# Optimization experiments

Hardware: AMD Instinct MI355X
Metric: run time of the kernel (lower is better)

## Reference

```python
import jax, jax.numpy as jnp
import numpy as np

NEG = -1e16  # matches torch masked_fill value
LN_EPS = 1e-5


def _gat_layer(h, mask, b):
    """h: [..., N, D]; mask: broadcastable bool [..., N, N]; b: broadcastable [..., D]."""
    scores = jnp.einsum('...nd,...md->...nm', h, h)
    scores = jnp.where(mask, scores, NEG)
    attn = jax.nn.softmax(scores, axis=-1)
    return jnp.einsum('...nm,...md->...nd', attn, h) + b


def setup_inputs() -> dict:
    key = jax.random.key(0)
    ks = jax.random.split(key, 6)
    B, N, C, H, D = 8, 2048, 64, 4, 64
    x = jax.random.normal(ks[0], (B, N, C), dtype=jnp.float32)
    graph = jax.random.randint(ks[1], (N, N), 0, 2, dtype=jnp.int32)
    # xavier_uniform-style scale for W: bound = sqrt(6/(fan_in+fan_out))
    bnd_h = float(np.sqrt(6.0 / (C + D)))
    Wh = jax.random.uniform(ks[2], (H, D, C), jnp.float32, -bnd_h, bnd_h)
    bh = jnp.zeros((H, D), jnp.float32)
    bnd_o = float(np.sqrt(6.0 / (H * D + D)))
    Wo = jax.random.uniform(ks[3], (D, H * D), jnp.float32, -bnd_o, bnd_o)
    bo = jnp.zeros((D,), jnp.float32)
    gamma = jnp.ones((D,), jnp.float32)
    beta = jnp.zeros((D,), jnp.float32)
    return {"x": x, "graph": graph, "Wh": Wh, "bh": bh, "Wo": Wo,
            "bo": bo, "gamma": gamma, "beta": beta}


def reference(x, graph, Wh, bh, Wo, bo, gamma, beta):
    B, N, C = x.shape
    H, D, _ = Wh.shape
    # graph = (graph + I) > 0
    mask = (graph + jnp.eye(N, dtype=graph.dtype)) > 0  # [N, N] bool
    # per-head linear projection: [B, H, N, D]
    h = jnp.einsum('bnc,hdc->bhnd', x, Wh)
    out_h = _gat_layer(h, mask[None, None], bh[None, :, None, :])  # [B,H,N,D]
    # torch.cat over heads along last dim == head-major reshape
    cat = jnp.transpose(out_h, (0, 2, 1, 3)).reshape(B, N, H * D)
    z = jax.nn.leaky_relu(cat, negative_slope=0.2)
    h2 = jnp.einsum('bnk,dk->bnd', z, Wo)  # [B, N, D]
    out2 = _gat_layer(h2, mask[None], bo)
    z2 = jax.nn.leaky_relu(out2, negative_slope=0.2)
    # LayerNorm over last dim
    mu = jnp.mean(z2, axis=-1, keepdims=True)
    var = jnp.mean(jnp.square(z2 - mu), axis=-1, keepdims=True)
    out = (z2 - mu) * jax.lax.rsqrt(var + LN_EPS) * gamma + beta
    return out  # dropout p=0.0 -> identity
```

## Files before the change

kernel.cpp:

```cpp
#include <hip/hip_runtime.h>

#define NN 2048
#define PITCH 72
#define MPITCH 264

typedef __attribute__((ext_vector_type(8))) _Float16 half8;
typedef __attribute__((ext_vector_type(4))) float floatx4;

static_assert(sizeof(half8) == 16, "");

#define MRINIT -3.0e38f

__device__ __forceinline__ unsigned short f2h(float f) {
    union { _Float16 h; unsigned short u; } v;
    v.h = (_Float16)f;
    return v.u;
}
__device__ __forceinline__ float h2f(unsigned short u) {
    union { unsigned short u; _Float16 h; } v;
    v.u = u;
    return (float)v.h;
}
__device__ __forceinline__ unsigned int pk2h(float a, float b) {
    union { __fp16 __attribute__((ext_vector_type(2))) h; unsigned int u; } v;
    v.h = __builtin_amdgcn_cvt_pkrtz(a, b);
    return v.u;
}
__device__ __forceinline__ void barrier_lds_only() {
    __asm__ __volatile__("" ::: "memory");
    __builtin_amdgcn_s_waitcnt(0xC07F);
    __builtin_amdgcn_s_barrier();
    __asm__ __volatile__("" ::: "memory");
}

__global__ __launch_bounds__(256) void mask_kernel(const int* __restrict__ graph,
                                                   unsigned int* __restrict__ mbits) {
    const int t = threadIdx.x;
    const int lane = t & 63;
    const int W = (blockIdx.x << 2) + (t >> 6);
    const int i = W >> 5;
    const int cb = W & 31;
    const int j = (cb << 6) + lane;
    const int g = graph[(size_t)i * NN + j];
    const unsigned long long bal = __ballot((g > 0) || (i == j));
    if (lane == 0)  mbits[(i << 6) + (cb << 1)]     = (unsigned int)bal;
    if (lane == 32) mbits[(i << 6) + (cb << 1) + 1] = (unsigned int)(bal >> 32);
}

__global__ __launch_bounds__(256) void proj_kernel(const float* __restrict__ x,
                                                   const float* __restrict__ Wh,
                                                   unsigned short* __restrict__ hout) {
    __shared__ float xs[16 * 64];
    __shared__ float wsh[64 * 65];
    const int t = threadIdx.x;
    const int pair = blockIdx.x >> 7;
    const int nt = blockIdx.x & 127;
    const int n0 = nt << 4;
    const int b = pair >> 2;
    const int hh = pair & 3;
    const float* xb = x + (((size_t)b * NN + n0) << 6);
    for (int i = t; i < 1024; i += 256) xs[i] = xb[i];
    const float* wb = Wh + (hh << 12);
    for (int i = t; i < 4096; i += 256) wsh[(i >> 6) * 65 + (i & 63)] = wb[i];
    __syncthreads();
    const int d = t & 63;
    const int q = t >> 6;
    float a0 = 0.f, a1 = 0.f, a2 = 0.f, a3 = 0.f;
    for (int c = 0; c < 64; ++c) {
        const float w = wsh[d * 65 + c];
        a0 += xs[(((q << 2) + 0) << 6) + c] * w;
        a1 += xs[(((q << 2) + 1) << 6) + c] * w;
        a2 += xs[(((q << 2) + 2) << 6) + c] * w;
        a3 += xs[(((q << 2) + 3) << 6) + c] * w;
    }
    unsigned short* ho = hout + (((size_t)pair * NN + n0 + (q << 2)) << 6) + d;
    ho[0]   = f2h(a0);
    ho[64]  = f2h(a1);
    ho[128] = f2h(a2);
    ho[192] = f2h(a3);
}

template <int QG, int OUTMODE>
__global__ __launch_bounds__(256) void gat_flash(const unsigned short* __restrict__ Hm,
                                                 const unsigned int* __restrict__ mbits,
                                                 const float* __restrict__ bias,
                                                 const int bias_mod,
                                                 const float* __restrict__ gamma,
                                                 const float* __restrict__ beta,
                                                 void* __restrict__ OutP,
                                                 float2* __restrict__ mlP) {
    __shared__ unsigned short Ks[2][64 * PITCH];
    __shared__ unsigned short Kts[2][64 * PITCH];
    __shared__ unsigned short Ps[4 * QG * 16 * PITCH];

    const int t = threadIdx.x;
    const int wave = t >> 6;
    const int lane = t & 63;
    const int quad = lane >> 4;
    const int m = lane & 15;

    const int qtbits = (QG == 2) ? 4 : 5;
    const int bid = blockIdx.x;
    const int qt = bid & ((1 << qtbits) - 1);
    const int split = (OUTMODE == 2) ? ((bid >> qtbits) & 1) : 0;
    const int mat = bid >> (qtbits + ((OUTMODE == 2) ? 1 : 0));
    const int q0 = qt << ((QG == 2) ? 7 : 6);
    const int nkt = (OUTMODE == 2) ? 16 : 32;
    const int kt0 = split * nkt;

    const unsigned short* Hb = Hm + ((size_t)mat << 17);
    const int wbase = q0 + wave * (16 * QG);

    const _Float16 LOG2E = (_Float16)1.44269504f;
    half8 bq0[QG], bq1[QG];
    int gq[QG];
#pragma unroll
    for (int g = 0; g < QG; ++g) {
        gq[g] = wbase + (g << 4) + m;
        bq0[g] = *(const half8*)(Hb + (gq[g] << 6) + (quad << 3)) * LOG2E;
        bq1[g] = *(const half8*)(Hb + (gq[g] << 6) + 32 + (quad << 3)) * LOG2E;
    }

    const int boff = (mat % bias_mod) << 6;
    const float bv0 = bias[boff + m];
    const float bv1 = bias[boff + 16 + m];
    const float bv2 = bias[boff + 32 + m];
    const float bv3 = bias[boff + 48 + m];

    const int p = t >> 3;
    const int cc = t & 7;
    const int jch = p >> 2;
    const int jo = (p & 3) << 1;

    float mr[QG], lr[QG];
    floatx4 O[QG][4];
#pragma unroll
    for (int g = 0; g < QG; ++g) {
        mr[g] = MRINIT;
        lr[g] = 0.f;
#pragma unroll
        for (int nt = 0; nt < 4; ++nt) O[g][nt] = floatx4{0.f, 0.f, 0.f, 0.f};
    }

    const int msw = m & 7;
    int psb[QG];
#pragma unroll
    for (int g = 0; g < QG; ++g) psb[g] = (wave * QG + g) * 1152 + m * PITCH;

    const unsigned short* kg0 = Hb + (((kt0 << 6) + (p << 1)) << 6) + (cc << 3);
    half8 ra = *(const half8*)(kg0);
    half8 rb = *(const half8*)(kg0 + 64);

    for (int it = 0; it < nkt; ++it) {
        const int kt = kt0 + it;
        unsigned short* KS = Ks[it & 1];
        unsigned short* KT = Kts[it & 1];
        *(half8*)(&KS[(p << 1) * PITCH + (cc << 3)]) = ra;
        *(half8*)(&KS[((p << 1) + 1) * PITCH + (cc << 3)]) = rb;
        union { half8 v; unsigned int u[4]; } kaU, kbU;
        kaU.v = ra;
        kbU.v = rb;
#pragma unroll
        for (int c = 0; c < 4; ++c) {
            const unsigned int ua = kaU.u[c];
            const unsigned int ub = kbU.u[c];
            const unsigned int lo = __builtin_amdgcn_perm(ub, ua, 0x05040100);
            const unsigned int hi = __builtin_amdgcn_perm(ub, ua, 0x07060302);
            const int d0 = (cc << 3) + (c << 1);
            const int pos = (((jch + cc) & 7) << 3) + jo;
            *(unsigned int*)(&KT[d0 * PITCH + pos]) = lo;
            *(unsigned int*)(&KT[(d0 + 1) * PITCH + pos]) = hi;
        }
        const int ktn = kt0 + ((it + 1) & (nkt - 1));
        const unsigned short* kgn = Hb + (((ktn << 6) + (p << 1)) << 6) + (cc << 3);
        ra = *(const half8*)(kgn);
        rb = *(const half8*)(kgn + 64);

        barrier_lds_only();

        floatx4 a[QG][4];
#pragma unroll
        for (int jt = 0; jt < 4; ++jt) {
            const half8 k0 = *(const half8*)(&KS[((jt << 4) + m) * PITCH + (quad << 3)]);
            const half8 k1 = *(const half8*)(&KS[((jt << 4) + m) * PITCH + 32 + (quad << 3)]);
#pragma unroll
            for (int g = 0; g < QG; ++g) {
                floatx4 z = {0.f, 0.f, 0.f, 0.f};
                z = __builtin_amdgcn_mfma_f32_16x16x32_f16(k0, bq0[g], z, 0, 0, 0);
                z = __builtin_amdgcn_mfma_f32_16x16x32_f16(k1, bq1[g], z, 0, 0, 0);
                a[g][jt] = z;
            }
        }

#pragma unroll
        for (int g = 0; g < QG; ++g) {
            const int mrow = gq[g] << 6;
            const unsigned int w0 = mbits[mrow + (kt << 1)];
            const unsigned int w1 = mbits[mrow + (kt << 1) + 1];

            float tmx = MRINIT;
#pragma unroll
            for (int jt = 0; jt < 4; ++jt) {
                const unsigned int wv = (jt < 2) ? w0 : w1;
                const unsigned int bits = (wv >> (((jt & 1) << 4) + (quad << 2))) & 0xFu;
#pragma unroll
                for (int reg = 0; reg < 4; ++reg) {
                    const float v = ((bits >> reg) & 1u) ? a[g][jt][reg] : MRINIT;
                    a[g][jt][reg] = v;
                    tmx = fmaxf(tmx, v);
                }
            }
            tmx = fmaxf(tmx, __shfl_xor(tmx, 16));
            tmx = fmaxf(tmx, __shfl_xor(tmx, 32));
            const float mnew = fmaxf(mr[g], tmx);
            const float alpha = __builtin_amdgcn_exp2f(mr[g] - mnew);
            const bool need = __any(mnew > mr[g]);

            float psum = 0.f;
#pragma unroll
            for (int jt = 0; jt < 4; ++jt) {
                const float p0 = __builtin_amdgcn_exp2f(a[g][jt][0] - mnew);
                const float p1 = __builtin_amdgcn_exp2f(a[g][jt][1] - mnew);
                const float p2 = __builtin_amdgcn_exp2f(a[g][jt][2] - mnew);
                const float p3 = __builtin_amdgcn_exp2f(a[g][jt][3] - mnew);
                psum += (p0 + p1) + (p2 + p3);
                const int ch = (jt << 1) + (quad >> 1);
                *(uint2*)(&Ps[psb[g] + (((ch + msw) & 7) << 3) + ((quad & 1) << 2)]) =
                    make_uint2(pk2h(p0, p1), pk2h(p2, p3));
            }
            psum += __shfl_xor(psum, 16);
            psum += __shfl_xor(psum, 32);
            lr[g] = lr[g] * alpha + psum;
            mr[g] = mnew;

            if (need) {
                const float aO0 = __shfl(alpha, (quad << 2) + 0);
                const float aO1 = __shfl(alpha, (quad << 2) + 1);
                const float aO2 = __shfl(alpha, (quad << 2) + 2);
                const float aO3 = __shfl(alpha, (quad << 2) + 3);
#pragma unroll
                for (int nt = 0; nt < 4; ++nt) {
                    O[g][nt][0] *= aO0;
                    O[g][nt][1] *= aO1;
                    O[g][nt][2] *= aO2;
                    O[g][nt][3] *= aO3;
                }
            }
        }

        __builtin_amdgcn_wave_barrier();
        __asm__ __volatile__("" ::: "memory");

        half8 pa0[QG], pa1[QG];
#pragma unroll
        for (int g = 0; g < QG; ++g) {
            pa0[g] = *(const half8*)(&Ps[psb[g] + (((quad + msw) & 7) << 3)]);
            pa1[g] = *(const half8*)(&Ps[psb[g] + (((4 + quad + msw) & 7) << 3)]);
        }
#pragma unroll
        for (int nt = 0; nt < 4; ++nt) {
            const int d = (nt << 4) + m;
            const int sw = (d >> 3) & 7;
            const half8 v0 = *(const half8*)(&KT[d * PITCH + (((quad + sw) & 7) << 3)]);
            const half8 v1 = *(const half8*)(&KT[d * PITCH + (((4 + quad + sw) & 7) << 3)]);
#pragma unroll
            for (int g = 0; g < QG; ++g) {
                O[g][nt] = __builtin_amdgcn_mfma_f32_16x16x32_f16(pa0[g], v0, O[g][nt], 0, 0, 0);
                O[g][nt] = __builtin_amdgcn_mfma_f32_16x16x32_f16(pa1[g], v1, O[g][nt], 0, 0, 0);
            }
        }
    }

    if (OUTMODE == 2) {
        float* Ob = (float*)OutP +
                    ((((size_t)(split << 3) + mat) * NN + wbase + (quad << 2)) << 6) + m;
#pragma unroll
        for (int reg = 0; reg < 4; ++reg)
#pragma unroll
            for (int nt = 0; nt < 4; ++nt)
                Ob[(reg << 6) + (nt << 4)] = O[0][nt][reg];
        if (lane < 16)
            mlP[((size_t)(split << 3) + mat) * NN + wbase + m] = make_float2(mr[0], lr[0]);
        return;
    }

    float g0, g1, g2, g3, be0, be1, be2, be3;
    if (OUTMODE == 1) {
        g0 = gamma[m]; g1 = gamma[16 + m]; g2 = gamma[32 + m]; g3 = gamma[48 + m];
        be0 = beta[m]; be1 = beta[16 + m]; be2 = beta[32 + m]; be3 = beta[48 + m];
    }
#pragma unroll
    for (int g = 0; g < QG; ++g) {
        const float l0 = 1.f / __shfl(lr[g], (quad << 2) + 0);
        const float l1 = 1.f / __shfl(lr[g], (quad << 2) + 1);
        const float l2 = 1.f / __shfl(lr[g], (quad << 2) + 2);
        const float l3 = 1.f / __shfl(lr[g], (quad << 2) + 3);
        const size_t obase = (((size_t)mat * NN + wbase + (g << 4) + (quad << 2)) << 6) + m;
#pragma unroll
        for (int reg = 0; reg < 4; ++reg) {
            const float li = (reg == 0) ? l0 : (reg == 1) ? l1 : (reg == 2) ? l2 : l3;
            float z0 = O[g][0][reg] * li + bv0;
            float z1 = O[g][1][reg] * li + bv1;
            float z2 = O[g][2][reg] * li + bv2;
            float z3 = O[g][3][reg] * li + bv3;
            z0 = (z0 > 0.f) ? z0 : 0.2f * z0;
            z1 = (z1 > 0.f) ? z1 : 0.2f * z1;
            z2 = (z2 > 0.f) ? z2 : 0.2f * z2;
            z3 = (z3 > 0.f) ? z3 : 0.2f * z3;
            if (OUTMODE == 0) {
                unsigned short* op = (unsigned short*)OutP + obase + ((size_t)reg << 6);
                op[0] = f2h(z0); op[16] = f2h(z1); op[32] = f2h(z2); op[48] = f2h(z3);
            } else {
                float s = ((z0 + z1) + (z2 + z3));
                float sq = ((z0 * z0 + z1 * z1) + (z2 * z2 + z3 * z3));
#pragma unroll
                for (int off = 1; off < 16; off <<= 1) {
                    s += __shfl_xor(s, off);
                    sq += __shfl_xor(sq, off);
                }
                const float mu = s * 0.015625f;
                float var = sq * 0.015625f - mu * mu;
                var = fmaxf(var, 0.f);
                const float rstd = rsqrtf(var + 1e-5f);
                float* op = (float*)OutP + obase + ((size_t)reg << 6);
                op[0]  = (z0 - mu) * rstd * g0 + be0;
                op[16] = (z1 - mu) * rstd * g1 + be1;
                op[32] = (z2 - mu) * rstd * g2 + be2;
                op[48] = (z3 - mu) * rstd * g3 + be3;
            }
        }
    }
}

__global__ __launch_bounds__(256) void mix_gemm(const unsigned short* __restrict__ oh,
                                                const float* __restrict__ Wo,
                                                unsigned short* __restrict__ h2) {
    __shared__ unsigned short zs[64 * MPITCH];
    __shared__ unsigned short wsm[64 * MPITCH];
    const int t = threadIdx.x;
    const int b = blockIdx.x >> 5;
    const int n0 = (blockIdx.x & 31) << 6;
    for (int i = t; i < 2048; i += 256) {
        const int hh = i >> 9;
        const int r = (i >> 3) & 63;
        const int d8 = i & 7;
        const half8 v = *(const half8*)(oh + ((((size_t)b << 2) + hh) * NN + n0 + r) * 64 + (d8 << 3));
        *(half8*)(&zs[r * MPITCH + (hh << 6) + (d8 << 3)]) = v;
    }
    for (int i = t; i < 2048; i += 256) {
        const int d = i >> 5;
        const int k0 = (i & 31) << 3;
        const float4 f0 = *(const float4*)(Wo + (d << 8) + k0);
        const float4 f1 = *(const float4*)(Wo + (d << 8) + k0 + 4);
        uint4 pk;
        pk.x = pk2h(f0.x, f0.y);
        pk.y = pk2h(f0.z, f0.w);
        pk.z = pk2h(f1.x, f1.y);
        pk.w = pk2h(f1.z, f1.w);
        *(uint4*)(&wsm[d * MPITCH + k0]) = pk;
    }
    __syncthreads();
    const int wave = t >> 6;
    const int m = t & 15;
    const int quad = (t >> 4) & 3;
    const int ar = (wave << 4) + m;
    floatx4 acc[4] = {{0.f, 0.f, 0.f, 0.f}, {0.f, 0.f, 0.f, 0.f},
                      {0.f, 0.f, 0.f, 0.f}, {0.f, 0.f, 0.f, 0.f}};
#pragma unroll
    for (int chunk = 0; chunk < 8; ++chunk) {
        const int k0 = chunk << 5;
        const half8 af = *(const half8*)(&zs[ar * MPITCH + k0 + (quad << 3)]);
#pragma unroll
        for (int nt = 0; nt < 4; ++nt) {
            const half8 bf = *(const half8*)(&wsm[((nt << 4) + m) * MPITCH + k0 + (quad << 3)]);
            acc[nt] = __builtin_amdgcn_mfma_f32_16x16x32_f16(af, bf, acc[nt], 0, 0, 0);
        }
    }
    unsigned short* hp = h2 + (((size_t)b * NN + n0 + (wave << 4) + (quad << 2)) << 6) + m;
#pragma unroll
    for (int reg = 0; reg < 4; ++reg)
#pragma unroll
        for (int nt = 0; nt < 4; ++nt)
            hp[(reg << 6) + (nt << 4)] = f2h(acc[nt][reg]);
}

__global__ __launch_bounds__(256) void combine_ln(const float* __restrict__ Opart,
                                                  const float2* __restrict__ ml,
                                                  const float* __restrict__ bo,
                                                  const float* __restrict__ gamma,
                                                  const float* __restrict__ beta,
                                                  float* __restrict__ out) {
    const int t = threadIdx.x;
    const int lane = t & 63;
    const int widx = (blockIdx.x << 2) + (t >> 6);
    const size_t r0 = (size_t)widx;
    const float2 s0 = ml[r0];
    const float2 s1 = ml[(size_t)(NN * 8) + r0];
    const float mm = fmaxf(s0.x, s1.x);
    const float c0 = __builtin_amdgcn_exp2f(s0.x - mm);
    const float c1 = __builtin_amdgcn_exp2f(s1.x - mm);
    const float l = s0.y * c0 + s1.y * c1;
    const float o0 = Opart[(r0 << 6) + lane];
    const float o1 = Opart[(((size_t)(NN * 8) + r0) << 6) + lane];
    float v = (o0 * c0 + o1 * c1) / l + bo[lane];
    v = (v > 0.f) ? v : 0.2f * v;
    float s = v;
    float sq = v * v;
#pragma unroll
    for (int off = 1; off < 64; off <<= 1) {
        s += __shfl_xor(s, off);
        sq += __shfl_xor(sq, off);
    }
    const float mu = s * 0.015625f;
    float var = sq * 0.015625f - mu * mu;
    var = fmaxf(var, 0.f);
    const float rstd = rsqrtf(var + 1e-5f);
    out[(r0 << 6) + lane] = (v - mu) * rstd * gamma[lane] + beta[lane];
}

extern "C" void kernel_launch(void* const* d_in, const int* in_sizes, int n_in,
                              void* d_out, int out_size, void* d_ws, size_t ws_size,
                              hipStream_t stream) {
    const float* x     = (const float*)d_in[0];
    const int*   graph = (const int*)d_in[1];
    const float* Wh    = (const float*)d_in[2];
    const float* bh    = (const float*)d_in[3];
    const float* Wo    = (const float*)d_in[4];
    const float* bo    = (const float*)d_in[5];
    const float* gamma = (const float*)d_in[6];
    const float* beta  = (const float*)d_in[7];
    float* out = (float*)d_out;

    char* ws = (char*)d_ws;
    unsigned int* mbits = (unsigned int*)ws;
    unsigned short* h   = (unsigned short*)(ws + 0x080000);
    unsigned short* oh  = (unsigned short*)(ws + 0x880000);
    unsigned short* h2  = (unsigned short*)(ws + 0x080000);
    float2* ml          = (float2*)(ws + 0x280000);
    float* Opart        = (float*)(ws + 0x880000);

    mask_kernel<<<16384, 256, 0, stream>>>(graph, mbits);
    proj_kernel<<<4096, 256, 0, stream>>>(x, Wh, h);
    gat_flash<2, 0><<<512, 256, 0, stream>>>(h, mbits, bh, 4, nullptr, nullptr, oh, nullptr);
    mix_gemm<<<256, 256, 0, stream>>>(oh, Wo, h2);
    gat_flash<1, 2><<<512, 256, 0, stream>>>(h2, mbits, bo, 1, nullptr, nullptr, Opart, ml);
    combine_ln<<<4096, 256, 0, stream>>>(Opart, ml, bo, gamma, beta, out);
}
```

Before: 219.8 us.

## Replace scalar projection kernel with fp16 MFMA GEMM and unpad P tile

Rewrites the per-head input projection as an MFMA-based GEMM: each block loads 64 rows of x and all four heads' weights into shared memory as fp16, and each wave computes one head with 16x16x32 MFMA instructions. The grid shrinks from 4096 to 256 blocks and x is read once per block for all heads instead of once per head. Separately, the P staging buffer in the attention kernel drops its padded pitch of 72 for a pitch of 64, which saves shared memory but may add bank conflicts unless the existing swizzle covers it. Converting x and W to fp16 before the projection changes rounding relative to the fp32 accumulation used before.

```diff
diff --git a/kernel.cpp b/kernel.cpp
--- a/kernel.cpp
+++ b/kernel.cpp
@@ -47,37 +47,68 @@
     if (lane == 32) mbits[(i << 6) + (cb << 1) + 1] = (unsigned int)(bal >> 32);
 }
 
-__global__ __launch_bounds__(256) void proj_kernel(const float* __restrict__ x,
-                                                   const float* __restrict__ Wh,
-                                                   unsigned short* __restrict__ hout) {
-    __shared__ float xs[16 * 64];
-    __shared__ float wsh[64 * 65];
+__global__ __launch_bounds__(256) void proj_gemm(const float* __restrict__ x,
+                                                 const float* __restrict__ Wh,
+                                                 unsigned short* __restrict__ hout) {
+    __shared__ unsigned short xs[64 * PITCH];
+    __shared__ unsigned short wh[4 * 64 * PITCH];
     const int t = threadIdx.x;
-    const int pair = blockIdx.x >> 7;
-    const int nt = blockIdx.x & 127;
-    const int n0 = nt << 4;
-    const int b = pair >> 2;
-    const int hh = pair & 3;
-    const float* xb = x + (((size_t)b * NN + n0) << 6);
-    for (int i = t; i < 1024; i += 256) xs[i] = xb[i];
-    const float* wb = Wh + (hh << 12);
-    for (int i = t; i < 4096; i += 256) wsh[(i >> 6) * 65 + (i & 63)] = wb[i];
+    const int b = blockIdx.x >> 5;
+    const int n0 = (blockIdx.x & 31) << 6;
+    for (int i = t; i < 512; i += 256) {
+        const int r = i >> 3, c8 = (i & 7) << 3;
+        const float* xp = x + (((size_t)b * NN + n0 + r) << 6) + c8;
+        const float4 f0 = *(const float4*)(xp);
+        const float4 f1 = *(const float4*)(xp + 4);
+        uint4 pk;
+        pk.x = pk2h(f0.x, f0.y); pk.y = pk2h(f0.z, f0.w);
+        pk.z = pk2h(f1.x, f1.y); pk.w = pk2h(f1.z, f1.w);
+        *(uint4*)(&xs[r * PITCH + c8]) = pk;
+    }
+    for (int i = t; i < 2048; i += 256) {
+        const int hd = i >> 3, c8 = (i & 7) << 3;
+        const float* wp = Wh + ((size_t)hd << 6) + c8;
+        const float4 f0 = *(const float4*)(wp);
+        const float4 f1 = *(const float4*)(wp + 4);
+        uint4 pk;
+        pk.x = pk2h(f0.x, f0.y); pk.y = pk2h(f0.z, f0.w);
+        pk.z = pk2h(f1.x, f1.y); pk.w = pk2h(f1.z, f1.w);
+        *(uint4*)(&wh[hd * PITCH + c8]) = pk;
+    }
     __syncthreads();
-    const int d = t & 63;
-    const int q = t >> 6;
-    float a0 = 0.f, a1 = 0.f, a2 = 0.f, a3 = 0.f;
-    for (int c = 0; c < 64; ++c) {
-        const float w = wsh[d * 65 + c];
-        a0 += xs[(((q << 2) + 0) << 6) + c] * w;
-        a1 += xs[(((q << 2) + 1) << 6) + c] * w;
-        a2 += xs[(((q << 2) + 2) << 6) + c] * w;
-        a3 += xs[(((q << 2) + 3) << 6) + c] * w;
-    }
-    unsigned short* ho = hout + (((size_t)pair * NN + n0 + (q << 2)) << 6) + d;
-    ho[0]   = f2h(a0);
-    ho[64]  = f2h(a1);
-    ho[128] = f2h(a2);
-    ho[192] = f2h(a3);
+    const int wave = t >> 6;
+    const int m = t & 15;
+    const int quad = (t >> 4) & 3;
+    half8 bf0[4], bf1[4];
+#pragma unroll
+    for (int nt = 0; nt < 4; ++nt) {
+        const int row = (wave << 6) + (nt << 4) + m;
+        bf0[nt] = *(const half8*)(&wh[row * PITCH + (quad << 3)]);
+        bf1[nt] = *(const half8*)(&wh[row * PITCH + 32 + (quad << 3)]);
+    }
+    floatx4 acc[4][4];
+#pragma unroll
+    for (int mt = 0; mt < 4; ++mt)
+#pragma unroll
+        for (int nt = 0; nt < 4; ++nt) acc[mt][nt] = floatx4{0.f, 0.f, 0.f, 0.f};
+#pragma unroll
+    for (int mt = 0; mt < 4; ++mt) {
+        const half8 a0 = *(const half8*)(&xs[((mt << 4) + m) * PITCH + (quad << 3)]);
+        const half8 a1 = *(const half8*)(&xs[((mt << 4) + m) * PITCH + 32 + (quad << 3)]);
+#pragma unroll
+        for (int nt = 0; nt < 4; ++nt) {
+            acc[mt][nt] = __builtin_amdgcn_mfma_f32_16x16x32_f16(a0, bf0[nt], acc[mt][nt], 0, 0, 0);
+            acc[mt][nt] = __builtin_amdgcn_mfma_f32_16x16x32_f16(a1, bf1[nt], acc[mt][nt], 0, 0, 0);
+        }
+    }
+    unsigned short* hp = hout + ((((size_t)(b << 2) + wave) * NN + n0) << 6) + m;
+#pragma unroll
+    for (int mt = 0; mt < 4; ++mt)
+#pragma unroll
+        for (int reg = 0; reg < 4; ++reg)
+#pragma unroll
+            for (int nt = 0; nt < 4; ++nt)
+                hp[(((mt << 4) + (quad << 2) + reg) << 6) + (nt << 4)] = f2h(acc[mt][nt][reg]);
 }
 
 template <int QG, int OUTMODE>
@@ -91,7 +122,7 @@
                                                  float2* __restrict__ mlP) {
     __shared__ unsigned short Ks[2][64 * PITCH];
     __shared__ unsigned short Kts[2][64 * PITCH];
-    __shared__ unsigned short Ps[4 * QG * 16 * PITCH];
+    __shared__ unsigned short Ps[4 * QG * 16 * 64];
 
     const int t = threadIdx.x;
     const int wave = t >> 6;
@@ -145,7 +176,7 @@
     const int msw = m & 7;
     int psb[QG];
 #pragma unroll
-    for (int g = 0; g < QG; ++g) psb[g] = (wave * QG + g) * 1152 + m * PITCH;
+    for (int g = 0; g < QG; ++g) psb[g] = (wave * QG + g) * 1024 + (m << 6);
 
     const unsigned short* kg0 = Hb + (((kt0 << 6) + (p << 1)) << 6) + (cc << 3);
     half8 ra = *(const half8*)(kg0);
@@ -440,7 +471,7 @@
     float* Opart        = (float*)(ws + 0x880000);
 
     mask_kernel<<<16384, 256, 0, stream>>>(graph, mbits);
-    proj_kernel<<<4096, 256, 0, stream>>>(x, Wh, h);
+    proj_gemm<<<256, 256, 0, stream>>>(x, Wh, h);
     gat_flash<2, 0><<<512, 256, 0, stream>>>(h, mbits, bh, 4, nullptr, nullptr, oh, nullptr);
     mix_gemm<<<256, 256, 0, stream>>>(oh, Wo, h2);
     gat_flash<1, 2><<<512, 256, 0, stream>>>(h2, mbits, bo, 1, nullptr, nullptr, Opart, ml);
```

Result: faster. 206.0 us (-6.3%).
